# Kernel optimization log

Hardware: AMD Instinct MI355X
Metric: run time of the kernel (lower is better)

The kernel has to match this reference:

```python
import jax, jax.numpy as jnp
import numpy as np
import math

B, T, D, H = 4, 2048, 1024, 16
DH = D // H

def setup_inputs() -> dict:
    key = jax.random.key(0)
    ks = jax.random.split(key, 12)
    s = 1.0 / math.sqrt(D)
    inp = {
        'q': jax.random.normal(ks[0], (B, T, D), jnp.float32),
        'k': jax.random.normal(ks[1], (B, T, D), jnp.float32),
        'v': jax.random.normal(ks[2], (B, T, D), jnp.float32),
        # causal attn_mask [B, Tq, Tk]; all-keep padding mask [B,1,1,Tk]
        'attn_mask': jnp.broadcast_to(jnp.tril(jnp.ones((T, T), jnp.bool_)), (B, T, T)),
        'key_keep_mask': jnp.ones((B, 1, 1, T), jnp.bool_),
        'wq_w': jax.random.normal(ks[3], (D, D), jnp.float32) * s,
        'wq_b': jnp.zeros((D,), jnp.float32),
        'wk_w': jax.random.normal(ks[4], (D, D), jnp.float32) * s,
        'wk_b': jnp.zeros((D,), jnp.float32),
        'wv_w': jax.random.normal(ks[5], (D, D), jnp.float32) * s,
        'wv_b': jnp.zeros((D,), jnp.float32),
        'wo_w': jax.random.normal(ks[6], (D, D), jnp.float32) * s,
        'wo_b': jnp.zeros((D,), jnp.float32),
    }
    return inp

def reference(q, k, v, attn_mask, key_keep_mask, wq_w, wq_b, wk_w, wk_b, wv_w, wv_b, wo_w, wo_b):
    # projections (torch Linear: x @ W^T + b)
    Q = (q @ wq_w.T + wq_b).reshape(B, -1, H, DH).transpose(0, 2, 1, 3)  # [B,H,Tq,DH]
    K = (k @ wk_w.T + wk_b).reshape(B, -1, H, DH).transpose(0, 2, 1, 3)
    V = (v @ wv_w.T + wv_b).reshape(B, -1, H, DH).transpose(0, 2, 1, 3)
    scores = jnp.einsum('bhqd,bhkd->bhqk', Q, K) / math.sqrt(DH)
    neg_inf = jnp.array(-jnp.inf, scores.dtype)
    scores = jnp.where(attn_mask[:, None, :, :], scores, neg_inf)
    scores = jnp.where(key_keep_mask, scores, neg_inf)
    attn = jax.nn.softmax(scores, axis=-1)  # dropout p=0 -> identity
    out = jnp.einsum('bhqk,bhkd->bhqd', attn, V)
    out = out.transpose(0, 2, 1, 3).reshape(B, -1, D)
    return out @ wo_w.T + wo_b
```

## Files before the change

### kernel.cpp

```cpp
#include <hip/hip_runtime.h>
#include <cstdint>
#include <cstddef>


typedef float f32x4 __attribute__((ext_vector_type(4)));
typedef short bf16x8 __attribute__((ext_vector_type(8)));
typedef float fltx4 __attribute__((ext_vector_type(4)));
typedef unsigned short u16x4 __attribute__((ext_vector_type(4)));

#define GLOBAL_AS __attribute__((address_space(1)))
#define LDS_AS __attribute__((address_space(3)))

__device__ __forceinline__ unsigned short f2bf(float f) {
    union { float f; unsigned int u; } x;
    x.f = f;
    unsigned int u = x.u;
    unsigned int r = (u + 0x7FFFu + ((u >> 16) & 1u)) >> 16;
    return (unsigned short)r;
}

__device__ __forceinline__ unsigned int pack_trunc(float a, float b) {
    union { float f; unsigned int u; } x, y;
    x.f = a; y.f = b;
    return (x.u >> 16) | (y.u & 0xFFFF0000u);
}

__global__ __launch_bounds__(256) void cast_all_kernel(
    const float* __restrict__ q, const float* __restrict__ k, const float* __restrict__ v,
    const float* __restrict__ wq, const float* __restrict__ wk,
    const float* __restrict__ wv, const float* __restrict__ wo,
    unsigned short* __restrict__ dst)
{
    const size_t SEG = 8388608;
    const size_t WSEG = 1048576;
    size_t i = ((size_t)blockIdx.x * 256 + threadIdx.x) * 4;
    const float* src;
    size_t off;
    if (i < SEG)               { src = q;  off = i; }
    else if (i < 2 * SEG)      { src = k;  off = i - SEG; }
    else if (i < 3 * SEG)      { src = v;  off = i - 2 * SEG; }
    else if (i < 3 * SEG + WSEG)     { src = wq; off = i - 3 * SEG; }
    else if (i < 3 * SEG + 2 * WSEG) { src = wk; off = i - 3 * SEG - WSEG; }
    else if (i < 3 * SEG + 3 * WSEG) { src = wv; off = i - 3 * SEG - 2 * WSEG; }
    else                             { src = wo; off = i - 3 * SEG - 3 * WSEG; }
    fltx4 val = *(const fltx4*)(src + off);
    u16x4 o;
    o[0] = f2bf(val[0]);
    o[1] = f2bf(val[1]);
    o[2] = f2bf(val[2]);
    o[3] = f2bf(val[3]);
    *(u16x4*)(dst + i) = o;
}

__global__ __launch_bounds__(256, 2) void qkv_gemm_kernel(
    const unsigned short* __restrict__ X,
    const unsigned short* __restrict__ Wc,
    const float* __restrict__ bq, const float* __restrict__ bk,
    const float* __restrict__ bv,
    unsigned short* __restrict__ Outs,
    float qscale)
{
    const int z = blockIdx.y;
    const unsigned short* A  = X  + (size_t)z * 8388608;
    const unsigned short* Bw = Wc + (size_t)z * 1048576;
    const float* bias = (z == 0) ? bq : (z == 1) ? bk : bv;
    unsigned short* outp = Outs + (size_t)z * 8388608;
    const float scale = (z == 0) ? qscale : 1.0f;
    const bool vmode = (z == 2);

    __shared__ __align__(16) unsigned short lds[3 * 12288];

    const int tid = threadIdx.x;
    const int w = tid >> 6, lane = tid & 63;
    const int quad = lane >> 4, l16 = lane & 15;
    const int wr = w >> 1, wc = w & 1;

    const int lin = blockIdx.x;
    const int r_ = lin & 7, s_ = lin >> 3;
    const int bm = (r_ * 4 + (s_ & 3)) * 256;
    const int bn = (s_ >> 2) * 128;

    const int rq = lane >> 2;
    const int cq = lane & 3;

    auto stageA = [&](int kt, int buf, int j) {
        unsigned short* lA = lds + buf * 12288;
        int r0 = w * 64 + j * 16;
        int row = r0 + rq;
        int csw = cq ^ ((row >> 1) & 3);
        __builtin_amdgcn_global_load_lds(
            (const GLOBAL_AS unsigned int*)(A + (size_t)(bm + row) * 1024 + kt * 32 + csw * 8),
            (LDS_AS unsigned int*)(lA + r0 * 32), 16, 0, 0);
    };
    auto stageB = [&](int kt, int buf, int j) {
        unsigned short* lB = lds + buf * 12288 + 8192;
        int r0 = w * 32 + j * 16;
        int row = r0 + rq;
        int csw = cq ^ ((row >> 1) & 3);
        __builtin_amdgcn_global_load_lds(
            (const GLOBAL_AS unsigned int*)(Bw + (size_t)(bn + row) * 1024 + kt * 32 + csw * 8),
            (LDS_AS unsigned int*)(lB + r0 * 32), 16, 0, 0);
    };

    f32x4 acc[8][4] = {};

    stageA(0, 0, 0); stageA(0, 0, 1); stageA(0, 0, 2); stageA(0, 0, 3);
    stageB(0, 0, 0); stageB(0, 0, 1);
    stageA(1, 1, 0); stageA(1, 1, 1); stageA(1, 1, 2); stageA(1, 1, 3);
    stageB(1, 1, 0); stageB(1, 1, 1);
    asm volatile("s_waitcnt vmcnt(6)" ::: "memory");
    __builtin_amdgcn_s_barrier();

    bf16x8 af[8], bfr[4];

    for (int kt = 0; kt < 32; ++kt) {
        const int cur = kt % 3;
        const int nxt = (kt + 2) % 3;
        const bool pre = (kt < 30);
        const unsigned short* lA = lds + cur * 12288;
        const unsigned short* lB = lA + 8192;

#pragma unroll
        for (int mi = 0; mi < 4; ++mi) {
            int row = wr * 128 + mi * 16 + l16;
            af[mi] = *(const bf16x8*)(lA + row * 32 + ((quad ^ ((row >> 1) & 3)) * 8));
        }
#pragma unroll
        for (int ni = 0; ni < 4; ++ni) {
            int row = wc * 64 + ni * 16 + l16;
            bfr[ni] = *(const bf16x8*)(lB + row * 32 + ((quad ^ ((row >> 1) & 3)) * 8));
        }
        if (pre) { stageA(kt + 2, nxt, 0); stageA(kt + 2, nxt, 1); stageB(kt + 2, nxt, 0); }

        __builtin_amdgcn_s_barrier();
        asm volatile("s_waitcnt lgkmcnt(0)" ::: "memory");
        __builtin_amdgcn_sched_barrier(0);
        __builtin_amdgcn_s_setprio(1);
#pragma unroll
        for (int mi = 0; mi < 4; ++mi)
#pragma unroll
            for (int ni = 0; ni < 4; ++ni)
                acc[mi][ni] = __builtin_amdgcn_mfma_f32_16x16x32_bf16(
                    af[mi], bfr[ni], acc[mi][ni], 0, 0, 0);
        __builtin_amdgcn_s_setprio(0);
        __builtin_amdgcn_sched_barrier(0);
        __builtin_amdgcn_s_barrier();

#pragma unroll
        for (int mi = 4; mi < 8; ++mi) {
            int row = wr * 128 + mi * 16 + l16;
            af[mi] = *(const bf16x8*)(lA + row * 32 + ((quad ^ ((row >> 1) & 3)) * 8));
        }
        if (pre) { stageA(kt + 2, nxt, 2); stageA(kt + 2, nxt, 3); stageB(kt + 2, nxt, 1); }

        __builtin_amdgcn_s_barrier();
        asm volatile("s_waitcnt lgkmcnt(0)" ::: "memory");
        __builtin_amdgcn_sched_barrier(0);
        __builtin_amdgcn_s_setprio(1);
#pragma unroll
        for (int mi = 4; mi < 8; ++mi)
#pragma unroll
            for (int ni = 0; ni < 4; ++ni)
                acc[mi][ni] = __builtin_amdgcn_mfma_f32_16x16x32_bf16(
                    af[mi], bfr[ni], acc[mi][ni], 0, 0, 0);
        __builtin_amdgcn_s_setprio(0);
        __builtin_amdgcn_sched_barrier(0);

        if (kt < 30)       asm volatile("s_waitcnt vmcnt(6)" ::: "memory");
        else if (kt == 30) asm volatile("s_waitcnt vmcnt(0)" ::: "memory");
        if (kt < 31) __builtin_amdgcn_s_barrier();
    }

#pragma unroll
    for (int mi = 0; mi < 8; ++mi) {
        int rowb = bm + wr * 128 + mi * 16 + quad * 4;
#pragma unroll
        for (int ni = 0; ni < 4; ++ni) {
            int col = bn + wc * 64 + ni * 16 + l16;
            float bv_ = bias[col];
            if (!vmode) {
#pragma unroll
                for (int r = 0; r < 4; ++r) {
                    int m = rowb + r;
                    float vout = acc[mi][ni][r] + bv_;
                    vout *= scale;
                    int b = m >> 11, t = m & 2047, h = col >> 6, d = col & 63;
                    outp[((size_t)(b * 16 + h) * 2048 + t) * 64 + d] = f2bf(vout);
                }
            } else {
                u16x4 o;
#pragma unroll
                for (int r = 0; r < 4; ++r)
                    o[r] = f2bf(acc[mi][ni][r] + bv_);
                int b = rowb >> 11, t0 = rowb & 2047, h = col >> 6, d = col & 63;
                *(u16x4*)(outp + ((size_t)(b * 16 + h) * 64 + d) * 2048 + t0) = o;
            }
        }
    }
}

__global__ __launch_bounds__(256, 3) void out_gemm_kernel(
    const unsigned short* __restrict__ A,
    const unsigned short* __restrict__ Bw,
    const float* __restrict__ bias,
    float* __restrict__ outp)
{
    __shared__ __align__(16) unsigned short lds[3 * 8192];

    const int tid = threadIdx.x;
    const int w = tid >> 6, lane = tid & 63;
    const int quad = lane >> 4, l16 = lane & 15;
    const int wr = w >> 1, wc = w & 1;

    const int lin = blockIdx.x;
    const int r_ = lin & 7, s_ = lin >> 3;
    const int bm = (r_ * 8 + (s_ & 7)) * 128;
    const int bn = (s_ >> 3) * 128;

    const int rq = lane >> 2;
    const int cq = lane & 3;

    auto stageA = [&](int kt, int buf, int j) {
        unsigned short* lA = lds + buf * 8192;
        int r0 = w * 32 + j * 16;
        int row = r0 + rq;
        int csw = cq ^ ((row >> 1) & 3);
        __builtin_amdgcn_global_load_lds(
            (const GLOBAL_AS unsigned int*)(A + (size_t)(bm + row) * 1024 + kt * 32 + csw * 8),
            (LDS_AS unsigned int*)(lA + r0 * 32), 16, 0, 0);
    };
    auto stageB = [&](int kt, int buf, int j) {
        unsigned short* lB = lds + buf * 8192 + 4096;
        int r0 = w * 32 + j * 16;
        int row = r0 + rq;
        int csw = cq ^ ((row >> 1) & 3);
        __builtin_amdgcn_global_load_lds(
            (const GLOBAL_AS unsigned int*)(Bw + (size_t)(bn + row) * 1024 + kt * 32 + csw * 8),
            (LDS_AS unsigned int*)(lB + r0 * 32), 16, 0, 0);
    };

    f32x4 acc[4][4] = {};

    stageA(0, 0, 0); stageA(0, 0, 1); stageB(0, 0, 0); stageB(0, 0, 1);
    stageA(1, 1, 0); stageA(1, 1, 1); stageB(1, 1, 0); stageB(1, 1, 1);
    asm volatile("s_waitcnt vmcnt(4)" ::: "memory");
    __builtin_amdgcn_s_barrier();

    for (int kt = 0; kt < 32; ++kt) {
        const int cur = kt % 3;
        const int nxt = (kt + 2) % 3;
        const bool pre = (kt < 30);
        const unsigned short* lA = lds + cur * 8192;
        const unsigned short* lB = lA + 4096;

        bf16x8 af[4], bfr[4];
#pragma unroll
        for (int mi = 0; mi < 4; ++mi) {
            int row = wr * 64 + mi * 16 + l16;
            af[mi] = *(const bf16x8*)(lA + row * 32 + ((quad ^ ((row >> 1) & 3)) * 8));
        }
#pragma unroll
        for (int ni = 0; ni < 4; ++ni) {
            int row = wc * 64 + ni * 16 + l16;
            bfr[ni] = *(const bf16x8*)(lB + row * 32 + ((quad ^ ((row >> 1) & 3)) * 8));
        }
        if (pre) { stageA(kt + 2, nxt, 0); stageA(kt + 2, nxt, 1);
                   stageB(kt + 2, nxt, 0); stageB(kt + 2, nxt, 1); }

        __builtin_amdgcn_s_barrier();
        asm volatile("s_waitcnt lgkmcnt(0)" ::: "memory");
        __builtin_amdgcn_sched_barrier(0);
        __builtin_amdgcn_s_setprio(1);
#pragma unroll
        for (int mi = 0; mi < 4; ++mi)
#pragma unroll
            for (int ni = 0; ni < 4; ++ni)
                acc[mi][ni] = __builtin_amdgcn_mfma_f32_16x16x32_bf16(
                    af[mi], bfr[ni], acc[mi][ni], 0, 0, 0);
        __builtin_amdgcn_s_setprio(0);
        __builtin_amdgcn_sched_barrier(0);

        if (kt < 30)       asm volatile("s_waitcnt vmcnt(4)" ::: "memory");
        else if (kt == 30) asm volatile("s_waitcnt vmcnt(0)" ::: "memory");
        if (kt < 31) __builtin_amdgcn_s_barrier();
    }

#pragma unroll
    for (int mi = 0; mi < 4; ++mi) {
        int rowb = bm + wr * 64 + mi * 16 + quad * 4;
#pragma unroll
        for (int ni = 0; ni < 4; ++ni) {
            int col = bn + wc * 64 + ni * 16 + l16;
            float bv_ = bias[col];
#pragma unroll
            for (int r = 0; r < 4; ++r)
                outp[(size_t)(rowb + r) * 1024 + col] = acc[mi][ni][r] + bv_;
        }
    }
}

__global__ __launch_bounds__(256) void attn_kernel(
    const unsigned short* __restrict__ Qh,
    const unsigned short* __restrict__ Kh,
    const unsigned short* __restrict__ Vt,
    unsigned short* __restrict__ att)
{
    const int tid = threadIdx.x;
    const int w = tid >> 6, lane = tid & 63;
    const int qd = lane >> 4, l16 = lane & 15;
    const int bh = blockIdx.x;
    const int pairy = blockIdx.y;

    const unsigned short* Qp = Qh + (size_t)bh * 2048 * 64;
    const unsigned short* Kp = Kh + (size_t)bh * 2048 * 64;
    const unsigned short* Vp = Vt + (size_t)bh * 64 * 2048;
    const int b = bh >> 4, h = bh & 15;

    __shared__ __align__(16) unsigned short Kl[3][64 * 64];
    __shared__ __align__(16) unsigned short Vl[3][64 * 64];
    __shared__ __align__(16) unsigned short Pl[4][2][16 * 64];

    auto stage = [&](int kt, int buf) {
#pragma unroll
        for (int j = 0; j < 2; ++j) {
            int r = w * 16 + j * 8 + (lane >> 3);
            int c = (lane & 7) ^ (r & 7);
            __builtin_amdgcn_global_load_lds(
                (const GLOBAL_AS unsigned int*)(Kp + (size_t)(kt * 64 + r) * 64 + c * 8),
                (LDS_AS unsigned int*)(&Kl[buf][(w * 16 + j * 8) * 64]), 16, 0, 0);
            __builtin_amdgcn_global_load_lds(
                (const GLOBAL_AS unsigned int*)(Vp + (size_t)r * 2048 + kt * 64 + c * 8),
                (LDS_AS unsigned int*)(&Vl[buf][(w * 16 + j * 8) * 64]), 16, 0, 0);
        }
    };

    auto run_phase = [&](int qblk) {
        const int wqbase = qblk * 128 + w * 32;
        const int ktmax = 2 * qblk + 1;

        bf16x8 qa[2][2];
#pragma unroll
        for (int qt = 0; qt < 2; ++qt)
#pragma unroll
            for (int ks = 0; ks < 2; ++ks)
                qa[qt][ks] = *(const bf16x8*)(Qp + (size_t)(wqbase + qt * 16 + l16) * 64 + ks * 32 + qd * 8);

        float lp[2] = {0.0f, 0.0f};
        f32x4 O[2][4] = {};

        __builtin_amdgcn_s_barrier();
        stage(0, 0);
        stage(1, 1);

        for (int kt = 0; kt <= ktmax; ++kt) {
            if (kt < ktmax) asm volatile("s_waitcnt vmcnt(4)" ::: "memory");
            else            asm volatile("s_waitcnt vmcnt(0)" ::: "memory");
            __builtin_amdgcn_s_barrier();
            if (kt + 2 <= ktmax) stage(kt + 2, (kt + 2) % 3);

            if (kt * 64 <= wqbase + 31) {
                const unsigned short* kl = &Kl[kt % 3][0];
                const unsigned short* vl = &Vl[kt % 3][0];

                bf16x8 kf[4][2];
#pragma unroll
                for (int nt = 0; nt < 4; ++nt)
#pragma unroll
                    for (int ks = 0; ks < 2; ++ks)
                        kf[nt][ks] = *(const bf16x8*)(kl + (nt * 16 + l16) * 64 +
                                                      (((ks * 4 + qd) ^ (l16 & 7)) * 8));

                f32x4 S[2][4];
#pragma unroll
                for (int qt = 0; qt < 2; ++qt)
#pragma unroll
                    for (int nt = 0; nt < 4; ++nt) {
                        f32x4 a = {};
                        a = __builtin_amdgcn_mfma_f32_16x16x32_bf16(kf[nt][0], qa[qt][0], a, 0, 0, 0);
                        a = __builtin_amdgcn_mfma_f32_16x16x32_bf16(kf[nt][1], qa[qt][1], a, 0, 0, 0);
                        S[qt][nt] = a;
                    }

                if (kt * 64 + 63 > wqbase) {
#pragma unroll
                    for (int qt = 0; qt < 2; ++qt) {
                        int qrow = wqbase + qt * 16 + l16;
#pragma unroll
                        for (int nt = 0; nt < 4; ++nt) {
                            int kbase = kt * 64 + nt * 16 + qd * 4;
#pragma unroll
                            for (int r = 0; r < 4; ++r)
                                if (kbase + r > qrow) S[qt][nt][r] = -INFINITY;
                        }
                    }
                }

#pragma unroll
                for (int qt = 0; qt < 2; ++qt) {
                    float s0 = 0.0f;
#pragma unroll
                    for (int nt = 0; nt < 4; ++nt)
#pragma unroll
                        for (int r = 0; r < 4; ++r) {
                            float e = __builtin_amdgcn_exp2f(S[qt][nt][r]);
                            S[qt][nt][r] = e;
                            s0 += e;
                        }
                    lp[qt] += s0;
                }

#pragma unroll
                for (int qt = 0; qt < 2; ++qt) {
                    unsigned short* pw = &Pl[w][qt][0];
#pragma unroll
                    for (int nt = 0; nt < 4; ++nt) {
                        uint2 pv;
                        pv.x = pack_trunc(S[qt][nt][0], S[qt][nt][1]);
                        pv.y = pack_trunc(S[qt][nt][2], S[qt][nt][3]);
                        int chunk = (2 * nt + (qd >> 1)) ^ (l16 & 7);
                        *(uint2*)(pw + l16 * 64 + chunk * 8 + (qd & 1) * 4) = pv;
                    }
                }
                asm volatile("s_waitcnt lgkmcnt(0)" ::: "memory");

                bf16x8 pa[2][2];
#pragma unroll
                for (int qt = 0; qt < 2; ++qt)
#pragma unroll
                    for (int s = 0; s < 2; ++s)
                        pa[qt][s] = *(const bf16x8*)(&Pl[w][qt][0] + l16 * 64 +
                                                     (((s * 4 + qd) ^ (l16 & 7)) * 8));

                bf16x8 vf[2][4];
#pragma unroll
                for (int s = 0; s < 2; ++s)
#pragma unroll
                    for (int dh = 0; dh < 4; ++dh)
                        vf[s][dh] = *(const bf16x8*)(vl + (dh * 16 + l16) * 64 +
                                                     (((s * 4 + qd) ^ (l16 & 7)) * 8));
#pragma unroll
                for (int qt = 0; qt < 2; ++qt)
#pragma unroll
                    for (int dh = 0; dh < 4; ++dh) {
                        O[qt][dh] = __builtin_amdgcn_mfma_f32_16x16x32_bf16(pa[qt][0], vf[0][dh], O[qt][dh], 0, 0, 0);
                        O[qt][dh] = __builtin_amdgcn_mfma_f32_16x16x32_bf16(pa[qt][1], vf[1][dh], O[qt][dh], 0, 0, 0);
                    }
            }
        }

#pragma unroll
        for (int qt = 0; qt < 2; ++qt) {
            float lsum = lp[qt];
            lsum += __shfl_xor(lsum, 16, 64);
            lsum += __shfl_xor(lsum, 32, 64);
            float linv = 1.0f / lsum;
#pragma unroll
            for (int r = 0; r < 4; ++r) {
                float lC = __shfl(linv, qd * 4 + r, 64);
                int t = wqbase + qt * 16 + qd * 4 + r;
#pragma unroll
                for (int dh = 0; dh < 4; ++dh) {
                    size_t idx = (size_t)(b * 2048 + t) * 1024 + h * 64 + dh * 16 + l16;
                    att[idx] = f2bf(O[qt][dh][r] * lC);
                }
            }
        }
    };

    run_phase(15 - pairy);
    run_phase(pairy);
}

extern "C" void kernel_launch(void* const* d_in, const int* in_sizes, int n_in,
                              void* d_out, int out_size, void* d_ws, size_t ws_size,
                              hipStream_t stream)
{
    const float* q = (const float*)d_in[0];
    const float* k = (const float*)d_in[1];
    const float* v = (const float*)d_in[2];
    const float* wq_w = (const float*)d_in[5];
    const float* wq_b = (const float*)d_in[6];
    const float* wk_w = (const float*)d_in[7];
    const float* wk_b = (const float*)d_in[8];
    const float* wv_w = (const float*)d_in[9];
    const float* wv_b = (const float*)d_in[10];
    const float* wo_w = (const float*)d_in[11];
    const float* wo_b = (const float*)d_in[12];

    unsigned short* ws = (unsigned short*)d_ws;
    unsigned short* xq  = ws;
    unsigned short* wqc = ws + 25165824;
    unsigned short* woc = ws + 28311552;
    unsigned short* Qhp = ws + 29360128;
    unsigned short* Khp = ws + 37748736;
    unsigned short* Vtp = ws + 46137344;
    unsigned short* att = xq;

    (void)in_sizes; (void)n_in; (void)out_size; (void)ws_size;

    cast_all_kernel<<<28672, 256, 0, stream>>>(q, k, v, wq_w, wk_w, wv_w, wo_w, ws);

    qkv_gemm_kernel<<<dim3(256, 3), 256, 0, stream>>>(
        xq, wqc, wq_b, wk_b, wv_b, Qhp, 0.1803368801f);

    attn_kernel<<<dim3(64, 8), 256, 0, stream>>>(Qhp, Khp, Vtp, att);

    out_gemm_kernel<<<512, 256, 0, stream>>>(att, woc, wo_b, (float*)d_out);
}
```

Baseline: 346.7 us.

## Fuse fp32-to-bf16 activation cast into QKV GEMM A-tile loads

Removes the separate cast pass over q/k/v: the QKV GEMM now reads fp32 activations directly into registers, converts them with v_cvt_pk_bf16_f32, and writes them to swizzled LDS. This saves a full write and re-read of a 48MB bf16 intermediate. The GEMM tile drops from 256x128 to 128x128 with three blocks per CU, and the loop is restructured to one barrier per k-step. The output GEMM pipeline is reordered the same way. The activation conversion changes from the manual round-to-nearest-even to the hardware conversion. Loads now go through registers instead of direct-to-LDS, which adds VGPR pressure and exposes more load latency.

New measurement: 348.3 us. About the same (+0.5%).

```diff
diff --git a/kernel.cpp b/kernel.cpp
--- a/kernel.cpp
+++ b/kernel.cpp
@@ -19,30 +19,31 @@
     return (unsigned short)r;
 }
 
+__device__ __forceinline__ unsigned int cvtpk_bf16(float lo, float hi) {
+    unsigned int d;
+    asm("v_cvt_pk_bf16_f32 %0, %1, %2" : "=v"(d) : "v"(lo), "v"(hi));
+    return d;
+}
+
 __device__ __forceinline__ unsigned int pack_trunc(float a, float b) {
     union { float f; unsigned int u; } x, y;
     x.f = a; y.f = b;
     return (x.u >> 16) | (y.u & 0xFFFF0000u);
 }
 
-__global__ __launch_bounds__(256) void cast_all_kernel(
-    const float* __restrict__ q, const float* __restrict__ k, const float* __restrict__ v,
+__global__ __launch_bounds__(256) void wcast_kernel(
     const float* __restrict__ wq, const float* __restrict__ wk,
     const float* __restrict__ wv, const float* __restrict__ wo,
     unsigned short* __restrict__ dst)
 {
-    const size_t SEG = 8388608;
     const size_t WSEG = 1048576;
     size_t i = ((size_t)blockIdx.x * 256 + threadIdx.x) * 4;
     const float* src;
     size_t off;
-    if (i < SEG)               { src = q;  off = i; }
-    else if (i < 2 * SEG)      { src = k;  off = i - SEG; }
-    else if (i < 3 * SEG)      { src = v;  off = i - 2 * SEG; }
-    else if (i < 3 * SEG + WSEG)     { src = wq; off = i - 3 * SEG; }
-    else if (i < 3 * SEG + 2 * WSEG) { src = wk; off = i - 3 * SEG - WSEG; }
-    else if (i < 3 * SEG + 3 * WSEG) { src = wv; off = i - 3 * SEG - 2 * WSEG; }
-    else                             { src = wo; off = i - 3 * SEG - 3 * WSEG; }
+    if (i < WSEG)          { src = wq; off = i; }
+    else if (i < 2 * WSEG) { src = wk; off = i - WSEG; }
+    else if (i < 3 * WSEG) { src = wv; off = i - 2 * WSEG; }
+    else                   { src = wo; off = i - 3 * WSEG; }
     fltx4 val = *(const fltx4*)(src + off);
     u16x4 o;
     o[0] = f2bf(val[0]);
@@ -52,8 +53,9 @@
     *(u16x4*)(dst + i) = o;
 }
 
-__global__ __launch_bounds__(256, 2) void qkv_gemm_kernel(
-    const unsigned short* __restrict__ X,
+__global__ __launch_bounds__(256, 3) void qkv_gemm_kernel(
+    const float* __restrict__ q, const float* __restrict__ k,
+    const float* __restrict__ v,
     const unsigned short* __restrict__ Wc,
     const float* __restrict__ bq, const float* __restrict__ bk,
     const float* __restrict__ bv,
@@ -61,14 +63,14 @@
     float qscale)
 {
     const int z = blockIdx.y;
-    const unsigned short* A  = X  + (size_t)z * 8388608;
+    const float* A = (z == 0) ? q : (z == 1) ? k : v;
     const unsigned short* Bw = Wc + (size_t)z * 1048576;
     const float* bias = (z == 0) ? bq : (z == 1) ? bk : bv;
     unsigned short* outp = Outs + (size_t)z * 8388608;
     const float scale = (z == 0) ? qscale : 1.0f;
     const bool vmode = (z == 2);
 
-    __shared__ __align__(16) unsigned short lds[3 * 12288];
+    __shared__ __align__(16) unsigned short lds[3 * 8192];
 
     const int tid = threadIdx.x;
     const int w = tid >> 6, lane = tid & 63;
@@ -77,52 +79,77 @@
 
     const int lin = blockIdx.x;
     const int r_ = lin & 7, s_ = lin >> 3;
-    const int bm = (r_ * 4 + (s_ & 3)) * 256;
-    const int bn = (s_ >> 2) * 128;
+    const int bm = ((r_ << 3) | (s_ & 7)) * 128;
+    const int bn = (s_ >> 3) * 128;
 
     const int rq = lane >> 2;
     const int cq = lane & 3;
-
-    auto stageA = [&](int kt, int buf, int j) {
-        unsigned short* lA = lds + buf * 12288;
-        int r0 = w * 64 + j * 16;
-        int row = r0 + rq;
-        int csw = cq ^ ((row >> 1) & 3);
-        __builtin_amdgcn_global_load_lds(
-            (const GLOBAL_AS unsigned int*)(A + (size_t)(bm + row) * 1024 + kt * 32 + csw * 8),
-            (LDS_AS unsigned int*)(lA + r0 * 32), 16, 0, 0);
-    };
-    auto stageB = [&](int kt, int buf, int j) {
-        unsigned short* lB = lds + buf * 12288 + 8192;
-        int r0 = w * 32 + j * 16;
-        int row = r0 + rq;
-        int csw = cq ^ ((row >> 1) & 3);
-        __builtin_amdgcn_global_load_lds(
-            (const GLOBAL_AS unsigned int*)(Bw + (size_t)(bn + row) * 1024 + kt * 32 + csw * 8),
-            (LDS_AS unsigned int*)(lB + r0 * 32), 16, 0, 0);
-    };
-
-    f32x4 acc[8][4] = {};
-
-    stageA(0, 0, 0); stageA(0, 0, 1); stageA(0, 0, 2); stageA(0, 0, 3);
-    stageB(0, 0, 0); stageB(0, 0, 1);
-    stageA(1, 1, 0); stageA(1, 1, 1); stageA(1, 1, 2); stageA(1, 1, 3);
-    stageB(1, 1, 0); stageB(1, 1, 1);
-    asm volatile("s_waitcnt vmcnt(6)" ::: "memory");
-    __builtin_amdgcn_s_barrier();
-
-    bf16x8 af[8], bfr[4];
+    const int arow0 = w * 32;
+
+    fltx4 areg[2][2];
+
+    auto issueA = [&](int kt) {
+#pragma unroll
+        for (int s = 0; s < 2; ++s) {
+            const float* p = A + (size_t)(bm + arow0 + s * 16 + rq) * 1024 + kt * 32 + cq * 8;
+            areg[s][0] = *(const fltx4*)p;
+            areg[s][1] = *(const fltx4*)(p + 4);
+        }
+    };
+    auto writeA = [&](int buf) {
+        unsigned short* lA = lds + buf * 8192;
+#pragma unroll
+        for (int s = 0; s < 2; ++s) {
+            int row = arow0 + s * 16 + rq;
+            int chunk = cq ^ ((row >> 1) & 3);
+            uint4 pk;
+            pk.x = cvtpk_bf16(areg[s][0][0], areg[s][0][1]);
+            pk.y = cvtpk_bf16(areg[s][0][2], areg[s][0][3]);
+            pk.z = cvtpk_bf16(areg[s][1][0], areg[s][1][1]);
+            pk.w = cvtpk_bf16(areg[s][1][2], areg[s][1][3]);
+            *(uint4*)(lA + row * 32 + chunk * 8) = pk;
+        }
+    };
+    auto issueB = [&](int kt, int buf) {
+        unsigned short* lB = lds + buf * 8192 + 4096;
+#pragma unroll
+        for (int g = 0; g < 2; ++g) {
+            int r0 = w * 32 + g * 16;
+            int row = r0 + rq;
+            int csw = cq ^ ((row >> 1) & 3);
+            __builtin_amdgcn_global_load_lds(
+                (const GLOBAL_AS unsigned int*)(Bw + (size_t)(bn + row) * 1024 + kt * 32 + csw * 8),
+                (LDS_AS unsigned int*)(lB + r0 * 32), 16, 0, 0);
+        }
+    };
+
+    f32x4 acc[4][4] = {};
+
+    issueA(0); issueB(0, 0);
+    asm volatile("s_waitcnt vmcnt(2)" ::: "memory");
+    writeA(0);
+    issueA(1); issueB(1, 1);
 
     for (int kt = 0; kt < 32; ++kt) {
         const int cur = kt % 3;
-        const int nxt = (kt + 2) % 3;
-        const bool pre = (kt < 30);
-        const unsigned short* lA = lds + cur * 12288;
-        const unsigned short* lB = lA + 8192;
-
+        if (kt < 31) {
+            asm volatile("s_waitcnt vmcnt(2)" ::: "memory");
+            writeA((kt + 1) % 3);
+        } else {
+            asm volatile("s_waitcnt vmcnt(0)" ::: "memory");
+        }
+        asm volatile("s_waitcnt lgkmcnt(0)" ::: "memory");
+        __builtin_amdgcn_sched_barrier(0);
+        __builtin_amdgcn_s_barrier();
+        __builtin_amdgcn_sched_barrier(0);
+        if (kt < 30) { issueA(kt + 2); issueB(kt + 2, (kt + 2) % 3); }
+
+        const unsigned short* lA = lds + cur * 8192;
+        const unsigned short* lB = lA + 4096;
+        bf16x8 af[4], bfr[4];
 #pragma unroll
         for (int mi = 0; mi < 4; ++mi) {
-            int row = wr * 128 + mi * 16 + l16;
+            int row = wr * 64 + mi * 16 + l16;
             af[mi] = *(const bf16x8*)(lA + row * 32 + ((quad ^ ((row >> 1) & 3)) * 8));
         }
 #pragma unroll
@@ -130,11 +157,6 @@
             int row = wc * 64 + ni * 16 + l16;
             bfr[ni] = *(const bf16x8*)(lB + row * 32 + ((quad ^ ((row >> 1) & 3)) * 8));
         }
-        if (pre) { stageA(kt + 2, nxt, 0); stageA(kt + 2, nxt, 1); stageB(kt + 2, nxt, 0); }
-
-        __builtin_amdgcn_s_barrier();
-        asm volatile("s_waitcnt lgkmcnt(0)" ::: "memory");
-        __builtin_amdgcn_sched_barrier(0);
         __builtin_amdgcn_s_setprio(1);
 #pragma unroll
         for (int mi = 0; mi < 4; ++mi)
@@ -143,37 +165,11 @@
                 acc[mi][ni] = __builtin_amdgcn_mfma_f32_16x16x32_bf16(
                     af[mi], bfr[ni], acc[mi][ni], 0, 0, 0);
         __builtin_amdgcn_s_setprio(0);
-        __builtin_amdgcn_sched_barrier(0);
-        __builtin_amdgcn_s_barrier();
-
-#pragma unroll
-        for (int mi = 4; mi < 8; ++mi) {
-            int row = wr * 128 + mi * 16 + l16;
-            af[mi] = *(const bf16x8*)(lA + row * 32 + ((quad ^ ((row >> 1) & 3)) * 8));
-        }
-        if (pre) { stageA(kt + 2, nxt, 2); stageA(kt + 2, nxt, 3); stageB(kt + 2, nxt, 1); }
-
-        __builtin_amdgcn_s_barrier();
-        asm volatile("s_waitcnt lgkmcnt(0)" ::: "memory");
-        __builtin_amdgcn_sched_barrier(0);
-        __builtin_amdgcn_s_setprio(1);
-#pragma unroll
-        for (int mi = 4; mi < 8; ++mi)
-#pragma unroll
-            for (int ni = 0; ni < 4; ++ni)
-                acc[mi][ni] = __builtin_amdgcn_mfma_f32_16x16x32_bf16(
-                    af[mi], bfr[ni], acc[mi][ni], 0, 0, 0);
-        __builtin_amdgcn_s_setprio(0);
-        __builtin_amdgcn_sched_barrier(0);
-
-        if (kt < 30)       asm volatile("s_waitcnt vmcnt(6)" ::: "memory");
-        else if (kt == 30) asm volatile("s_waitcnt vmcnt(0)" ::: "memory");
-        if (kt < 31) __builtin_amdgcn_s_barrier();
     }
 
 #pragma unroll
-    for (int mi = 0; mi < 8; ++mi) {
-        int rowb = bm + wr * 128 + mi * 16 + quad * 4;
+    for (int mi = 0; mi < 4; ++mi) {
+        int rowb = bm + wr * 64 + mi * 16 + quad * 4;
 #pragma unroll
         for (int ni = 0; ni < 4; ++ni) {
             int col = bn + wc * 64 + ni * 16 + l16;
@@ -182,8 +178,7 @@
 #pragma unroll
                 for (int r = 0; r < 4; ++r) {
                     int m = rowb + r;
-                    float vout = acc[mi][ni][r] + bv_;
-                    vout *= scale;
+                    float vout = (acc[mi][ni][r] + bv_) * scale;
                     int b = m >> 11, t = m & 2047, h = col >> 6, d = col & 63;
                     outp[((size_t)(b * 16 + h) * 2048 + t) * 64 + d] = f2bf(vout);
                 }
@@ -214,45 +209,45 @@
 
     const int lin = blockIdx.x;
     const int r_ = lin & 7, s_ = lin >> 3;
-    const int bm = (r_ * 8 + (s_ & 7)) * 128;
+    const int bm = ((r_ << 3) | (s_ & 7)) * 128;
     const int bn = (s_ >> 3) * 128;
 
     const int rq = lane >> 2;
     const int cq = lane & 3;
 
-    auto stageA = [&](int kt, int buf, int j) {
+    auto stage = [&](int kt, int buf) {
         unsigned short* lA = lds + buf * 8192;
-        int r0 = w * 32 + j * 16;
-        int row = r0 + rq;
-        int csw = cq ^ ((row >> 1) & 3);
-        __builtin_amdgcn_global_load_lds(
-            (const GLOBAL_AS unsigned int*)(A + (size_t)(bm + row) * 1024 + kt * 32 + csw * 8),
-            (LDS_AS unsigned int*)(lA + r0 * 32), 16, 0, 0);
-    };
-    auto stageB = [&](int kt, int buf, int j) {
-        unsigned short* lB = lds + buf * 8192 + 4096;
-        int r0 = w * 32 + j * 16;
-        int row = r0 + rq;
-        int csw = cq ^ ((row >> 1) & 3);
-        __builtin_amdgcn_global_load_lds(
-            (const GLOBAL_AS unsigned int*)(Bw + (size_t)(bn + row) * 1024 + kt * 32 + csw * 8),
-            (LDS_AS unsigned int*)(lB + r0 * 32), 16, 0, 0);
+        unsigned short* lB = lA + 4096;
+#pragma unroll
+        for (int g = 0; g < 2; ++g) {
+            int r0 = w * 32 + g * 16;
+            int row = r0 + rq;
+            int csw = cq ^ ((row >> 1) & 3);
+            __builtin_amdgcn_global_load_lds(
+                (const GLOBAL_AS unsigned int*)(A + (size_t)(bm + row) * 1024 + kt * 32 + csw * 8),
+                (LDS_AS unsigned int*)(lA + r0 * 32), 16, 0, 0);
+            __builtin_amdgcn_global_load_lds(
+                (const GLOBAL_AS unsigned int*)(Bw + (size_t)(bn + row) * 1024 + kt * 32 + csw * 8),
+                (LDS_AS unsigned int*)(lB + r0 * 32), 16, 0, 0);
+        }
     };
 
     f32x4 acc[4][4] = {};
 
-    stageA(0, 0, 0); stageA(0, 0, 1); stageB(0, 0, 0); stageB(0, 0, 1);
-    stageA(1, 1, 0); stageA(1, 1, 1); stageB(1, 1, 0); stageB(1, 1, 1);
-    asm volatile("s_waitcnt vmcnt(4)" ::: "memory");
-    __builtin_amdgcn_s_barrier();
+    stage(0, 0);
+    stage(1, 1);
 
     for (int kt = 0; kt < 32; ++kt) {
         const int cur = kt % 3;
-        const int nxt = (kt + 2) % 3;
-        const bool pre = (kt < 30);
+        if (kt < 31) asm volatile("s_waitcnt vmcnt(4)" ::: "memory");
+        else         asm volatile("s_waitcnt vmcnt(0)" ::: "memory");
+        __builtin_amdgcn_sched_barrier(0);
+        __builtin_amdgcn_s_barrier();
+        __builtin_amdgcn_sched_barrier(0);
+        if (kt < 30) stage(kt + 2, (kt + 2) % 3);
+
         const unsigned short* lA = lds + cur * 8192;
         const unsigned short* lB = lA + 4096;
-
         bf16x8 af[4], bfr[4];
 #pragma unroll
         for (int mi = 0; mi < 4; ++mi) {
@@ -264,12 +259,6 @@
             int row = wc * 64 + ni * 16 + l16;
             bfr[ni] = *(const bf16x8*)(lB + row * 32 + ((quad ^ ((row >> 1) & 3)) * 8));
         }
-        if (pre) { stageA(kt + 2, nxt, 0); stageA(kt + 2, nxt, 1);
-                   stageB(kt + 2, nxt, 0); stageB(kt + 2, nxt, 1); }
-
-        __builtin_amdgcn_s_barrier();
-        asm volatile("s_waitcnt lgkmcnt(0)" ::: "memory");
-        __builtin_amdgcn_sched_barrier(0);
         __builtin_amdgcn_s_setprio(1);
 #pragma unroll
         for (int mi = 0; mi < 4; ++mi)
@@ -278,11 +267,6 @@
                 acc[mi][ni] = __builtin_amdgcn_mfma_f32_16x16x32_bf16(
                     af[mi], bfr[ni], acc[mi][ni], 0, 0, 0);
         __builtin_amdgcn_s_setprio(0);
-        __builtin_amdgcn_sched_barrier(0);
-
-        if (kt < 30)       asm volatile("s_waitcnt vmcnt(4)" ::: "memory");
-        else if (kt == 30) asm volatile("s_waitcnt vmcnt(0)" ::: "memory");
-        if (kt < 31) __builtin_amdgcn_s_barrier();
     }
 
 #pragma unroll
@@ -498,10 +482,10 @@
 
     (void)in_sizes; (void)n_in; (void)out_size; (void)ws_size;
 
-    cast_all_kernel<<<28672, 256, 0, stream>>>(q, k, v, wq_w, wk_w, wv_w, wo_w, ws);
-
-    qkv_gemm_kernel<<<dim3(256, 3), 256, 0, stream>>>(
-        xq, wqc, wq_b, wk_b, wv_b, Qhp, 0.1803368801f);
+    wcast_kernel<<<4096, 256, 0, stream>>>(wq_w, wk_w, wv_w, wo_w, wqc);
+
+    qkv_gemm_kernel<<<dim3(512, 3), 256, 0, stream>>>(
+        q, k, v, wqc, wq_b, wk_b, wv_b, Qhp, 0.1803368801f);
 
     attn_kernel<<<dim3(64, 8), 256, 0, stream>>>(Qhp, Khp, Vtp, att);
 
```
